# Kernel tuning notes

Hardware: AMD Instinct MI355X
Metric: run time of the kernel (lower is better)

## Reference

```python
import jax, jax.numpy as jnp
import numpy as np

NY, NX = 800, 700  # BEV grid from voxel_feature_shape[2], voxel_feature_shape[3]
NCH = 2            # voxel_feature_shape[1] + 1 = occupancy + intensity


def setup_inputs() -> dict:
    key = jax.random.key(0)
    N, T, B = 200000, 32, 16
    k1, k2, k3, k4, k5 = jax.random.split(key, 5)
    vox_feats = jax.random.normal(k1, (N, T, 5), dtype=jnp.float32)
    num_points = jax.random.randint(k2, (N,), 1, T + 1, dtype=jnp.int32)
    b = jax.random.randint(k3, (N, 1), 0, B, dtype=jnp.int32)
    y = jax.random.randint(k4, (N, 1), 0, NY, dtype=jnp.int32)
    x = jax.random.randint(k5, (N, 1), 0, NX, dtype=jnp.int32)
    z = jnp.zeros((N, 1), dtype=jnp.int32)
    coords = jnp.concatenate([b, z, y, x], axis=1)  # [N, 4] = (batch, z, y, x)
    return {"vox_feats": vox_feats, "num_points": num_points,
            "coords": coords, "batch_size": B}


def reference(vox_feats, num_points, coords, batch_size):
    # intensity: mean over points per voxel, last feature channel -> [N]
    intensity = vox_feats.mean(axis=1)[:, -1]
    # occupancy value is 1.0 for every non-empty voxel (ones_like(num_points))
    # fuse the per-batch loop into one global scatter with batch-offset indices
    flat = (coords[:, 0].astype(jnp.int32) * (NY * NX)
            + coords[:, 2].astype(jnp.int32) * NX
            + coords[:, 3].astype(jnp.int32))  # [N]
    occ = jnp.zeros((batch_size * NY * NX,), dtype=vox_feats.dtype).at[flat].set(1.0)
    inten = jnp.zeros((batch_size * NY * NX,), dtype=vox_feats.dtype).at[flat].set(intensity)
    # [B, 2, NY, NX]
    return jnp.stack([occ.reshape(batch_size, NY, NX),
                      inten.reshape(batch_size, NY, NX)], axis=1)
```

## Files before the change

kernel.cpp:

```cpp
#include <hip/hip_runtime.h>
#include <hip/hip_bf16.h>


#define PX_NY 800
#define PX_NX 700
#define PX_T  32
#define PX_C  5

__global__ void __launch_bounds__(256)
pixor_intens_vote(const float* __restrict__ vox,
                  const int*   __restrict__ coords,
                  float*       __restrict__ intens,
                  int*         __restrict__ out_i,
                  int N, int P ) {
    int n = blockIdx.x * blockDim.x + threadIdx.x;
    if (n >= N) return;

    const float* row = vox + (size_t)n * (PX_T * PX_C) + (PX_C - 1);
    float s = 0.0f;
#pragma unroll
    for (int t = 0; t < PX_T; ++t) {
        s += row[t * PX_C];
    }
    intens[n] = s * (1.0f / (float)PX_T);

    int4 c = ((const int4*)coords)[n];
    int cell = c.x * (2 * P) + P + c.z * PX_NX + c.w;
    atomicMax(out_i + cell, n + 1);
}

__global__ void __launch_bounds__(256)
pixor_finalize(const int*   __restrict__ coords,
               const float* __restrict__ intens,
               float*       __restrict__ out,
               int N, int P) {
    int n = blockIdx.x * blockDim.x + threadIdx.x;
    if (n >= N) return;

    int4 c = ((const int4*)coords)[n];
    int base = c.x * (2 * P) + c.z * PX_NX + c.w;

    out[base] = 1.0f;

    int* ip = (int*)out + base + P;
    if (*ip == n + 1) {
        *(float*)ip = intens[n];
    }
}

extern "C" void kernel_launch(void* const* d_in, const int* in_sizes, int n_in,
                              void* d_out, int out_size, void* d_ws, size_t ws_size,
                              hipStream_t stream) {
    const float* vox    = (const float*)d_in[0];
    const int*   coords = (const int*)d_in[2];
    float* out = (float*)d_out;

    const int N = in_sizes[1];
    const int P = PX_NY * PX_NX;

    float* ws_int = (float*)d_ws;

    hipMemsetAsync(d_out, 0, (size_t)out_size * sizeof(float), stream);

    const int BLK = 256;
    const int grid = (N + BLK - 1) / BLK;

    pixor_intens_vote<<<grid, BLK, 0, stream>>>(vox, coords, ws_int, (int*)out, N, P);
    pixor_finalize  <<<grid, BLK, 0, stream>>>(coords, ws_int, out, N, P);
}
```

Measured before the change: 52.48 us.

## Fuse output zeroing with vectorized intensity reduction into one kernel

Replaces the memset with a custom kernel that zeroes the output using float4 stores, and has extra threads in the same launch compute per-voxel intensity means with float4 loads. The atomic vote moves to its own kernel, so the zeroing and the 128 MB voxel read overlap in a single bandwidth-bound launch. This adds a third launch and assumes out_size is divisible by 4 and that rows are 16-byte aligned.

```diff
diff --git a/kernel.cpp b/kernel.cpp
--- a/kernel.cpp
+++ b/kernel.cpp
@@ -8,22 +8,36 @@
 #define PX_C  5
 
 __global__ void __launch_bounds__(256)
-pixor_intens_vote(const float* __restrict__ vox,
-                  const int*   __restrict__ coords,
-                  float*       __restrict__ intens,
-                  int*         __restrict__ out_i,
-                  int N, int P ) {
+pixor_zero_intens(const float4* __restrict__ vox4,
+                  float4*       __restrict__ out4, int zq,
+                  float*        __restrict__ intens, int N) {
+    int i = blockIdx.x * blockDim.x + threadIdx.x;
+    if (i < zq) {
+        out4[i] = make_float4(0.f, 0.f, 0.f, 0.f);
+    } else {
+        int n = i - zq;
+        if (n < N) {
+            const float4* rp = vox4 + (size_t)n * (PX_T * PX_C / 4);
+            float s = 0.f;
+#pragma unroll
+            for (int g = 0; g < 8; ++g) {
+                float4 a = rp[g * 5 + 1];
+                float4 b = rp[g * 5 + 2];
+                float4 c = rp[g * 5 + 3];
+                float4 d = rp[g * 5 + 4];
+                s += (a.x + b.y) + (c.z + d.w);
+            }
+            intens[n] = s * (1.0f / (float)PX_T);
+        }
+    }
+}
+
+__global__ void __launch_bounds__(256)
+pixor_vote(const int* __restrict__ coords,
+           int*       __restrict__ out_i,
+           int N, int P) {
     int n = blockIdx.x * blockDim.x + threadIdx.x;
     if (n >= N) return;
-
-    const float* row = vox + (size_t)n * (PX_T * PX_C) + (PX_C - 1);
-    float s = 0.0f;
-#pragma unroll
-    for (int t = 0; t < PX_T; ++t) {
-        s += row[t * PX_C];
-    }
-    intens[n] = s * (1.0f / (float)PX_T);
-
     int4 c = ((const int4*)coords)[n];
     int cell = c.x * (2 * P) + P + c.z * PX_NX + c.w;
     atomicMax(out_i + cell, n + 1);
@@ -36,7 +50,6 @@
                int N, int P) {
     int n = blockIdx.x * blockDim.x + threadIdx.x;
     if (n >= N) return;
-
     int4 c = ((const int4*)coords)[n];
     int base = c.x * (2 * P) + c.z * PX_NX + c.w;
 
@@ -60,11 +73,14 @@
 
     float* ws_int = (float*)d_ws;
 
-    hipMemsetAsync(d_out, 0, (size_t)out_size * sizeof(float), stream);
+    const int BLK = 256;
 
-    const int BLK = 256;
+    const int zq    = out_size / 4;
+    const int total = zq + N;
+    pixor_zero_intens<<<(total + BLK - 1) / BLK, BLK, 0, stream>>>(
+        (const float4*)vox, (float4*)out, zq, ws_int, N);
+
     const int grid = (N + BLK - 1) / BLK;
-
-    pixor_intens_vote<<<grid, BLK, 0, stream>>>(vox, coords, ws_int, (int*)out, N, P);
-    pixor_finalize  <<<grid, BLK, 0, stream>>>(coords, ws_int, out, N, P);
+    pixor_vote<<<grid, BLK, 0, stream>>>(coords, (int*)out, N, P);
+    pixor_finalize<<<grid, BLK, 0, stream>>>(coords, ws_int, out, N, P);
 }
```

After: 56.27 us. 1.07x slower.
